# Kernel optimization log

Hardware: AMD Instinct MI355X
Metric: run time of the kernel (lower is better)

The kernel has to match this reference:

```python
import jax, jax.numpy as jnp
import numpy as np

ALPHA = 0.25
GAMMA = 2.0
FG_W = 13.0
BG_W = 1.0
DS = 8  # downsample_factor: boxes are in original image coords, masks at feature res


def setup_inputs() -> dict:
    key = jax.random.key(0)
    k1, k2, k3, k4 = jax.random.split(key, 4)
    B, N, C, H, W, M = 2, 6, 81, 112, 200, 20
    depth_logits = jax.random.normal(k1, (B, N, C, H, W), dtype=jnp.float32)
    depth_target = jax.random.randint(k2, (B, N, H, W), 0, C, dtype=jnp.int32)
    # (x, y, w, h) boxes in original image coords (~1600x900)
    xy = jax.random.uniform(k3, (B, N, M, 2)) * jnp.array([1400.0, 700.0], jnp.float32)
    wh = 20.0 + jax.random.uniform(k4, (B, N, M, 2)) * 180.0
    gt_bboxes_2d = jnp.concatenate([xy, wh], axis=-1).astype(jnp.float32)
    return {"depth_logits": depth_logits, "depth_target": depth_target,
            "gt_bboxes_2d": gt_bboxes_2d}


def _focal_loss(logits, target):
    # logits [BN, C, H, W], target [BN, H, W] -> per-pixel focal loss [BN, H, W]
    log_p = jax.nn.log_softmax(logits, axis=1)
    log_pt = jnp.take_along_axis(log_p, target[:, None].astype(jnp.int32), axis=1)[:, 0]
    pt = jnp.exp(log_pt)
    return -ALPHA * (1.0 - pt) ** GAMMA * log_pt


def _fg_mask(boxes, H, W):
    # boxes [BN, M, 4] = (x, y, w, h); rectangle fill at feature resolution
    x, y, w, h = boxes[..., 0], boxes[..., 1], boxes[..., 2], boxes[..., 3]
    u1 = jnp.floor(x / DS)
    v1 = jnp.floor(y / DS)
    u2 = jnp.ceil((x + w) / DS)
    v2 = jnp.ceil((y + h) / DS)
    xs = jnp.arange(W, dtype=jnp.float32)
    ys = jnp.arange(H, dtype=jnp.float32)
    in_x = (xs[None, None, :] >= u1[..., None]) & (xs[None, None, :] < u2[..., None])  # [BN,M,W]
    in_y = (ys[None, None, :] >= v1[..., None]) & (ys[None, None, :] < v2[..., None])  # [BN,M,H]
    return jnp.any(in_y[:, :, :, None] & in_x[:, :, None, :], axis=1)  # [BN,H,W]


def reference(depth_logits, depth_target, gt_bboxes_2d):
    B, N, C, H, W = depth_logits.shape
    logits = depth_logits.reshape(B * N, C, H, W)
    target = depth_target.reshape(B * N, H, W)
    loss = _focal_loss(logits, target)  # [BN, H, W]

    fg = _fg_mask(gt_bboxes_2d.reshape(B * N, -1, 4), H, W)
    bg = ~fg
    weights = jnp.where(fg, FG_W, BG_W).astype(loss.dtype)
    num_pixels = jnp.asarray(fg.size, loss.dtype)  # fg.sum() + bg.sum() == total pixels

    wloss = loss * weights
    fg_loss = jnp.where(fg, wloss, 0.0).sum() / num_pixels
    bg_loss = jnp.where(bg, wloss, 0.0).sum() / num_pixels
    return fg_loss + bg_loss
```

## Files before the change

kernel.cpp:

```cpp
#include <hip/hip_runtime.h>
#include <math.h>

namespace {
constexpr int Bc = 2, Nc = 6, Cc = 81, Hc = 112, Wc = 200, Mc = 20;
constexpr int BN   = Bc * Nc;
constexpr int HW   = Hc * Wc;
constexpr int NPIX = BN * HW;
constexpr float kAlpha = 0.25f;
constexpr float kFgW   = 13.0f;
constexpr float kBgW   = 1.0f;
constexpr float kInvDS = 0.125f;
}

__global__ __launch_bounds__(256) void ddn_loss_kernel(
    const float* __restrict__ logits,
    const int*   __restrict__ target,
    const float* __restrict__ boxes,
    float* __restrict__ out)
{
    const int tid  = blockIdx.x * 256 + threadIdx.x;
    const int pix0 = tid * 4;
    float local = 0.0f;

    if (pix0 < NPIX) {
        const int bn = pix0 / HW;
        const int hw = pix0 - bn * HW;
        const int h  = hw / Wc;
        const int w  = hw - h * Wc;

        const float4* lp =
            reinterpret_cast<const float4*>(logits + (size_t)bn * Cc * HW + hw);
        const int4 tg =
            *reinterpret_cast<const int4*>(target + (size_t)bn * HW + hw);

        float s0 = 0.f, s1 = 0.f, s2 = 0.f, s3 = 0.f;
        float x0 = 0.f, x1 = 0.f, x2 = 0.f, x3 = 0.f;
        #pragma unroll 3
        for (int c = 0; c < Cc; ++c) {
            const float4 v = lp[(size_t)c * (HW / 4)];
            s0 += __expf(v.x);
            s1 += __expf(v.y);
            s2 += __expf(v.z);
            s3 += __expf(v.w);
            if (c == tg.x) x0 = v.x;
            if (c == tg.y) x1 = v.y;
            if (c == tg.z) x2 = v.z;
            if (c == tg.w) x3 = v.w;
        }

        const float lp0 = x0 - __logf(s0);
        const float lp1 = x1 - __logf(s1);
        const float lp2 = x2 - __logf(s2);
        const float lp3 = x3 - __logf(s3);
        const float om0 = 1.f - __expf(lp0);
        const float om1 = 1.f - __expf(lp1);
        const float om2 = 1.f - __expf(lp2);
        const float om3 = 1.f - __expf(lp3);
        const float l0 = -kAlpha * om0 * om0 * lp0;
        const float l1 = -kAlpha * om1 * om1 * lp1;
        const float l2 = -kAlpha * om2 * om2 * lp2;
        const float l3 = -kAlpha * om3 * om3 * lp3;

        const float* bx = boxes + (size_t)bn * Mc * 4;
        bool f0 = false, f1 = false, f2 = false, f3 = false;
        const float hf  = (float)h;
        const float w0f = (float)w;
        const float w1f = w0f + 1.f, w2f = w0f + 2.f, w3f = w0f + 3.f;
        #pragma unroll
        for (int m = 0; m < Mc; ++m) {
            const float bxx = bx[m * 4 + 0];
            const float bxy = bx[m * 4 + 1];
            const float bxw = bx[m * 4 + 2];
            const float bxh = bx[m * 4 + 3];
            const float u1 = floorf(bxx * kInvDS);
            const float v1 = floorf(bxy * kInvDS);
            const float u2 = ceilf((bxx + bxw) * kInvDS);
            const float v2 = ceilf((bxy + bxh) * kInvDS);
            const bool iny = (hf >= v1) & (hf < v2);
            f0 |= iny & (w0f >= u1) & (w0f < u2);
            f1 |= iny & (w1f >= u1) & (w1f < u2);
            f2 |= iny & (w2f >= u1) & (w2f < u2);
            f3 |= iny & (w3f >= u1) & (w3f < u2);
        }

        local = l0 * (f0 ? kFgW : kBgW)
              + l1 * (f1 ? kFgW : kBgW)
              + l2 * (f2 ? kFgW : kBgW)
              + l3 * (f3 ? kFgW : kBgW);
    }

    #pragma unroll
    for (int off = 32; off > 0; off >>= 1)
        local += __shfl_down(local, off, 64);
    __shared__ float smem[4];
    const int lane = threadIdx.x & 63;
    const int wv   = threadIdx.x >> 6;
    if (lane == 0) smem[wv] = local;
    __syncthreads();
    if (threadIdx.x == 0) {
        const float bs = smem[0] + smem[1] + smem[2] + smem[3];
        atomicAdd(out, bs * (1.0f / (float)NPIX));
    }
}

extern "C" void kernel_launch(void* const* d_in, const int* in_sizes, int n_in,
                              void* d_out, int out_size, void* d_ws, size_t ws_size,
                              hipStream_t stream) {
    const float* logits = (const float*)d_in[0];
    const int*   target = (const int*)d_in[1];
    const float* boxes  = (const float*)d_in[2];
    float* out = (float*)d_out;

    hipMemsetAsync(out, 0, sizeof(float), stream);

    const int nthreads = NPIX / 4;
    const int blocks   = (nthreads + 255) / 256;
    ddn_loss_kernel<<<blocks, 256, 0, stream>>>(logits, target, boxes, out);
}
```

Measured before the change: 29.15 us.

## Split class reduction across waves and combine partial softmax sums in shared memory

```diff
diff --git a/kernel.cpp b/kernel.cpp
--- a/kernel.cpp
+++ b/kernel.cpp
@@ -3,9 +3,12 @@
 
 namespace {
 constexpr int Bc = 2, Nc = 6, Cc = 81, Hc = 112, Wc = 200, Mc = 20;
-constexpr int BN   = Bc * Nc;
-constexpr int HW   = Hc * Wc;
-constexpr int NPIX = BN * HW;
+constexpr int BN    = Bc * Nc;
+constexpr int HW    = Hc * Wc;
+constexpr int NPIX  = BN * HW;
+constexpr int NQUAD = NPIX / 4;
+constexpr int QPB   = 64;
+constexpr int NBLK  = NQUAD / QPB;
 constexpr float kAlpha = 0.25f;
 constexpr float kFgW   = 13.0f;
 constexpr float kBgW   = 1.0f;
@@ -18,89 +21,96 @@
     const float* __restrict__ boxes,
     float* __restrict__ out)
 {
-    const int tid  = blockIdx.x * 256 + threadIdx.x;
-    const int pix0 = tid * 4;
-    float local = 0.0f;
+    __shared__ float smem[4][QPB][9];
+    __shared__ float wsum[4];
 
-    if (pix0 < NPIX) {
-        const int bn = pix0 / HW;
-        const int hw = pix0 - bn * HW;
-        const int h  = hw / Wc;
-        const int w  = hw - h * Wc;
+    const int t    = threadIdx.x;
+    const int lane = t & 63;
+    const int y    = t >> 6;
 
-        const float4* lp =
-            reinterpret_cast<const float4*>(logits + (size_t)bn * Cc * HW + hw);
-        const int4 tg =
-            *reinterpret_cast<const int4*>(target + (size_t)bn * HW + hw);
+    const int quad = blockIdx.x * QPB + lane;
+    const int pix0 = quad * 4;
+    const int bn   = pix0 / HW;
+    const int hw   = pix0 - bn * HW;
 
-        float s0 = 0.f, s1 = 0.f, s2 = 0.f, s3 = 0.f;
-        float x0 = 0.f, x1 = 0.f, x2 = 0.f, x3 = 0.f;
-        #pragma unroll 3
-        for (int c = 0; c < Cc; ++c) {
-            const float4 v = lp[(size_t)c * (HW / 4)];
-            s0 += __expf(v.x);
-            s1 += __expf(v.y);
-            s2 += __expf(v.z);
-            s3 += __expf(v.w);
-            if (c == tg.x) x0 = v.x;
-            if (c == tg.y) x1 = v.y;
-            if (c == tg.z) x2 = v.z;
-            if (c == tg.w) x3 = v.w;
-        }
+    const float4* lp =
+        reinterpret_cast<const float4*>(logits + (size_t)bn * Cc * HW + hw);
+    const int4 tg =
+        *reinterpret_cast<const int4*>(target + (size_t)bn * HW + hw);
 
-        const float lp0 = x0 - __logf(s0);
-        const float lp1 = x1 - __logf(s1);
-        const float lp2 = x2 - __logf(s2);
-        const float lp3 = x3 - __logf(s3);
-        const float om0 = 1.f - __expf(lp0);
-        const float om1 = 1.f - __expf(lp1);
-        const float om2 = 1.f - __expf(lp2);
-        const float om3 = 1.f - __expf(lp3);
-        const float l0 = -kAlpha * om0 * om0 * lp0;
-        const float l1 = -kAlpha * om1 * om1 * lp1;
-        const float l2 = -kAlpha * om2 * om2 * lp2;
-        const float l3 = -kAlpha * om3 * om3 * lp3;
+    float s0 = 0.f, s1 = 0.f, s2 = 0.f, s3 = 0.f;
+    float x0 = 0.f, x1 = 0.f, x2 = 0.f, x3 = 0.f;
+    #pragma unroll 5
+    for (int i = 0; i < 20; ++i) {
+        const int c = y + i * 4;
+        const float4 v = lp[(size_t)c * (HW / 4)];
+        s0 += __expf(v.x);
+        s1 += __expf(v.y);
+        s2 += __expf(v.z);
+        s3 += __expf(v.w);
+        if (c == tg.x) x0 = v.x;
+        if (c == tg.y) x1 = v.y;
+        if (c == tg.z) x2 = v.z;
+        if (c == tg.w) x3 = v.w;
+    }
+    if (y == 0) {
+        const int c = 80;
+        const float4 v = lp[(size_t)c * (HW / 4)];
+        s0 += __expf(v.x);
+        s1 += __expf(v.y);
+        s2 += __expf(v.z);
+        s3 += __expf(v.w);
+        if (c == tg.x) x0 = v.x;
+        if (c == tg.y) x1 = v.y;
+        if (c == tg.z) x2 = v.z;
+        if (c == tg.w) x3 = v.w;
+    }
+    smem[y][lane][0] = s0; smem[y][lane][1] = s1;
+    smem[y][lane][2] = s2; smem[y][lane][3] = s3;
+    smem[y][lane][4] = x0; smem[y][lane][5] = x1;
+    smem[y][lane][6] = x2; smem[y][lane][7] = x3;
+    __syncthreads();
 
-        const float* bx = boxes + (size_t)bn * Mc * 4;
-        bool f0 = false, f1 = false, f2 = false, f3 = false;
-        const float hf  = (float)h;
-        const float w0f = (float)w;
-        const float w1f = w0f + 1.f, w2f = w0f + 2.f, w3f = w0f + 3.f;
-        #pragma unroll
-        for (int m = 0; m < Mc; ++m) {
-            const float bxx = bx[m * 4 + 0];
-            const float bxy = bx[m * 4 + 1];
-            const float bxw = bx[m * 4 + 2];
-            const float bxh = bx[m * 4 + 3];
-            const float u1 = floorf(bxx * kInvDS);
-            const float v1 = floorf(bxy * kInvDS);
-            const float u2 = ceilf((bxx + bxw) * kInvDS);
-            const float v2 = ceilf((bxy + bxh) * kInvDS);
-            const bool iny = (hf >= v1) & (hf < v2);
-            f0 |= iny & (w0f >= u1) & (w0f < u2);
-            f1 |= iny & (w1f >= u1) & (w1f < u2);
-            f2 |= iny & (w2f >= u1) & (w2f < u2);
-            f3 |= iny & (w3f >= u1) & (w3f < u2);
-        }
+    const int q = t >> 2;
+    const int p = t & 3;
+    const float s = smem[0][q][p]     + smem[1][q][p]
+                  + smem[2][q][p]     + smem[3][q][p];
+    const float x = smem[0][q][4 + p] + smem[1][q][4 + p]
+                  + smem[2][q][4 + p] + smem[3][q][4 + p];
 
-        local = l0 * (f0 ? kFgW : kBgW)
-              + l1 * (f1 ? kFgW : kBgW)
-              + l2 * (f2 ? kFgW : kBgW)
-              + l3 * (f3 ? kFgW : kBgW);
+    const int pixel = (blockIdx.x * QPB + q) * 4 + p;
+    const int bn2   = pixel / HW;
+    const int rem   = pixel - bn2 * HW;
+    const int h     = rem / Wc;
+    const int w     = rem - h * Wc;
+
+    const float lpt  = x - __logf(s);
+    const float om   = 1.f - __expf(lpt);
+    const float loss = -kAlpha * om * om * lpt;
+
+    const float* bx = boxes + (size_t)bn2 * Mc * 4;
+    bool fg = false;
+    const float hf = (float)h, wf = (float)w;
+    #pragma unroll
+    for (int m = 0; m < Mc; ++m) {
+        const float bxx = bx[m * 4 + 0];
+        const float bxy = bx[m * 4 + 1];
+        const float u1 = floorf(bxx * kInvDS);
+        const float v1 = floorf(bxy * kInvDS);
+        const float u2 = ceilf((bxx + bx[m * 4 + 2]) * kInvDS);
+        const float v2 = ceilf((bxy + bx[m * 4 + 3]) * kInvDS);
+        fg |= (hf >= v1) & (hf < v2) & (wf >= u1) & (wf < u2);
     }
+    float local = loss * (fg ? kFgW : kBgW);
 
     #pragma unroll
     for (int off = 32; off > 0; off >>= 1)
         local += __shfl_down(local, off, 64);
-    __shared__ float smem[4];
-    const int lane = threadIdx.x & 63;
-    const int wv   = threadIdx.x >> 6;
-    if (lane == 0) smem[wv] = local;
+    if ((t & 63) == 0) wsum[t >> 6] = local;
     __syncthreads();
-    if (threadIdx.x == 0) {
-        const float bs = smem[0] + smem[1] + smem[2] + smem[3];
-        atomicAdd(out, bs * (1.0f / (float)NPIX));
-    }
+    if (t == 0)
+        atomicAdd(out, (wsum[0] + wsum[1] + wsum[2] + wsum[3])
+                           * (1.0f / (float)NPIX));
 }
 
 extern "C" void kernel_launch(void* const* d_in, const int* in_sizes, int n_in,
@@ -113,7 +123,5 @@
 
     hipMemsetAsync(out, 0, sizeof(float), stream);
 
-    const int nthreads = NPIX / 4;
-    const int blocks   = (nthreads + 255) / 256;
-    ddn_loss_kernel<<<blocks, 256, 0, stream>>>(logits, target, boxes, out);
+    ddn_loss_kernel<<<NBLK, 256, 0, stream>>>(logits, target, boxes, out);
 }
```

Result: slower. 36.76 us (+26.1%).

## Double-buffer channel loads in registers and use single-wavefront blocks

Applied to the files above, without the earlier changes.

```diff
diff --git a/kernel.cpp b/kernel.cpp
--- a/kernel.cpp
+++ b/kernel.cpp
@@ -2,42 +2,58 @@
 #include <math.h>
 
 namespace {
-constexpr int Bc = 2, Nc = 6, Cc = 81, Hc = 112, Wc = 200, Mc = 20;
-constexpr int BN   = Bc * Nc;
-constexpr int HW   = Hc * Wc;
-constexpr int NPIX = BN * HW;
+constexpr int Cc = 81, Hc = 112, Wc = 200, Mc = 20;
+constexpr int BN    = 12;
+constexpr int HW    = Hc * Wc;
+constexpr int NPIX  = BN * HW;
+constexpr int NQUAD = NPIX / 4;
+constexpr int TPB   = 64;
+constexpr int NBLK  = NQUAD / TPB;
 constexpr float kAlpha = 0.25f;
 constexpr float kFgW   = 13.0f;
 constexpr float kBgW   = 1.0f;
 constexpr float kInvDS = 0.125f;
 }
 
-__global__ __launch_bounds__(256) void ddn_loss_kernel(
+__global__ __launch_bounds__(64) void ddn_loss_kernel(
     const float* __restrict__ logits,
     const int*   __restrict__ target,
     const float* __restrict__ boxes,
     float* __restrict__ out)
 {
-    const int tid  = blockIdx.x * 256 + threadIdx.x;
+    const int tid  = blockIdx.x * TPB + threadIdx.x;
     const int pix0 = tid * 4;
-    float local = 0.0f;
+    const int bn   = pix0 / HW;
+    const int hw   = pix0 - bn * HW;
+    const int h    = hw / Wc;
+    const int w    = hw - h * Wc;
 
-    if (pix0 < NPIX) {
-        const int bn = pix0 / HW;
-        const int hw = pix0 - bn * HW;
-        const int h  = hw / Wc;
-        const int w  = hw - h * Wc;
+    const float4* lp =
+        reinterpret_cast<const float4*>(logits + (size_t)bn * Cc * HW + hw);
+    const int4 tg =
+        *reinterpret_cast<const int4*>(target + (size_t)bn * HW + hw);
 
-        const float4* lp =
-            reinterpret_cast<const float4*>(logits + (size_t)bn * Cc * HW + hw);
-        const int4 tg =
-            *reinterpret_cast<const int4*>(target + (size_t)bn * HW + hw);
+    float s0 = 0.f, s1 = 0.f, s2 = 0.f, s3 = 0.f;
+    float x0 = 0.f, x1 = 0.f, x2 = 0.f, x3 = 0.f;
 
-        float s0 = 0.f, s1 = 0.f, s2 = 0.f, s3 = 0.f;
-        float x0 = 0.f, x1 = 0.f, x2 = 0.f, x3 = 0.f;
-        #pragma unroll 3
-        for (int c = 0; c < Cc; ++c) {
-            const float4 v = lp[(size_t)c * (HW / 4)];
+    float4 vv[2][9];
+    #pragma unroll
+    for (int j = 0; j < 9; ++j)
+        vv[0][j] = lp[(size_t)j * (HW / 4)];
+
+    #pragma unroll
+    for (int b = 0; b < 9; ++b) {
+        const int cur = b & 1;
+        if (b < 8) {
+            const int nxt = cur ^ 1;
+            #pragma unroll
+            for (int j = 0; j < 9; ++j)
+                vv[nxt][j] = lp[(size_t)((b + 1) * 9 + j) * (HW / 4)];
+        }
+        #pragma unroll
+        for (int j = 0; j < 9; ++j) {
+            const int c = b * 9 + j;
+            const float4 v = vv[cur][j];
             s0 += __expf(v.x);
             s1 += __expf(v.y);
             s2 += __expf(v.z);
@@ -47,60 +63,51 @@
             if (c == tg.z) x2 = v.z;
             if (c == tg.w) x3 = v.w;
         }
+    }
 
-        const float lp0 = x0 - __logf(s0);
-        const float lp1 = x1 - __logf(s1);
-        const float lp2 = x2 - __logf(s2);
-        const float lp3 = x3 - __logf(s3);
-        const float om0 = 1.f - __expf(lp0);
-        const float om1 = 1.f - __expf(lp1);
-        const float om2 = 1.f - __expf(lp2);
-        const float om3 = 1.f - __expf(lp3);
-        const float l0 = -kAlpha * om0 * om0 * lp0;
-        const float l1 = -kAlpha * om1 * om1 * lp1;
-        const float l2 = -kAlpha * om2 * om2 * lp2;
-        const float l3 = -kAlpha * om3 * om3 * lp3;
+    const float lp0 = x0 - __logf(s0);
+    const float lp1 = x1 - __logf(s1);
+    const float lp2 = x2 - __logf(s2);
+    const float lp3 = x3 - __logf(s3);
+    const float om0 = 1.f - __expf(lp0);
+    const float om1 = 1.f - __expf(lp1);
+    const float om2 = 1.f - __expf(lp2);
+    const float om3 = 1.f - __expf(lp3);
+    const float l0 = -kAlpha * om0 * om0 * lp0;
+    const float l1 = -kAlpha * om1 * om1 * lp1;
+    const float l2 = -kAlpha * om2 * om2 * lp2;
+    const float l3 = -kAlpha * om3 * om3 * lp3;
 
-        const float* bx = boxes + (size_t)bn * Mc * 4;
-        bool f0 = false, f1 = false, f2 = false, f3 = false;
-        const float hf  = (float)h;
-        const float w0f = (float)w;
-        const float w1f = w0f + 1.f, w2f = w0f + 2.f, w3f = w0f + 3.f;
-        #pragma unroll
-        for (int m = 0; m < Mc; ++m) {
-            const float bxx = bx[m * 4 + 0];
-            const float bxy = bx[m * 4 + 1];
-            const float bxw = bx[m * 4 + 2];
-            const float bxh = bx[m * 4 + 3];
-            const float u1 = floorf(bxx * kInvDS);
-            const float v1 = floorf(bxy * kInvDS);
-            const float u2 = ceilf((bxx + bxw) * kInvDS);
-            const float v2 = ceilf((bxy + bxh) * kInvDS);
-            const bool iny = (hf >= v1) & (hf < v2);
-            f0 |= iny & (w0f >= u1) & (w0f < u2);
-            f1 |= iny & (w1f >= u1) & (w1f < u2);
-            f2 |= iny & (w2f >= u1) & (w2f < u2);
-            f3 |= iny & (w3f >= u1) & (w3f < u2);
-        }
+    const float* bx = boxes + (size_t)bn * Mc * 4;
+    bool f0 = false, f1 = false, f2 = false, f3 = false;
+    const float hf  = (float)h;
+    const float w0f = (float)w;
+    const float w1f = w0f + 1.f, w2f = w0f + 2.f, w3f = w0f + 3.f;
+    #pragma unroll
+    for (int m = 0; m < Mc; ++m) {
+        const float bxx = bx[m * 4 + 0];
+        const float bxy = bx[m * 4 + 1];
+        const float u1 = floorf(bxx * kInvDS);
+        const float v1 = floorf(bxy * kInvDS);
+        const float u2 = ceilf((bxx + bx[m * 4 + 2]) * kInvDS);
+        const float v2 = ceilf((bxy + bx[m * 4 + 3]) * kInvDS);
+        const bool iny = (hf >= v1) & (hf < v2);
+        f0 |= iny & (w0f >= u1) & (w0f < u2);
+        f1 |= iny & (w1f >= u1) & (w1f < u2);
+        f2 |= iny & (w2f >= u1) & (w2f < u2);
+        f3 |= iny & (w3f >= u1) & (w3f < u2);
+    }
 
-        local = l0 * (f0 ? kFgW : kBgW)
-              + l1 * (f1 ? kFgW : kBgW)
-              + l2 * (f2 ? kFgW : kBgW)
-              + l3 * (f3 ? kFgW : kBgW);
-    }
+    float local = l0 * (f0 ? kFgW : kBgW)
+                + l1 * (f1 ? kFgW : kBgW)
+                + l2 * (f2 ? kFgW : kBgW)
+                + l3 * (f3 ? kFgW : kBgW);
 
     #pragma unroll
     for (int off = 32; off > 0; off >>= 1)
         local += __shfl_down(local, off, 64);
-    __shared__ float smem[4];
-    const int lane = threadIdx.x & 63;
-    const int wv   = threadIdx.x >> 6;
-    if (lane == 0) smem[wv] = local;
-    __syncthreads();
-    if (threadIdx.x == 0) {
-        const float bs = smem[0] + smem[1] + smem[2] + smem[3];
-        atomicAdd(out, bs * (1.0f / (float)NPIX));
-    }
+    if (threadIdx.x == 0)
+        atomicAdd(out, local * (1.0f / (float)NPIX));
 }
 
 extern "C" void kernel_launch(void* const* d_in, const int* in_sizes, int n_in,
@@ -113,7 +120,5 @@
 
     hipMemsetAsync(out, 0, sizeof(float), stream);
 
-    const int nthreads = NPIX / 4;
-    const int blocks   = (nthreads + 255) / 256;
-    ddn_loss_kernel<<<blocks, 256, 0, stream>>>(logits, target, boxes, out);
+    ddn_loss_kernel<<<NBLK, TPB, 0, stream>>>(logits, target, boxes, out);
 }
```

After: 37.62 us. 29.0% more time.
